# Performance work log

Measured on AMD Instinct MI355X. Metric: run time of the kernel, lower is better.

The kernel has to match this reference:

```python
import jax, jax.numpy as jnp
import numpy as np

D = 512  # input_size
H = 512  # hidden_size

def _linear_init(key, out_f, in_f):
    k1, k2 = jax.random.split(key)
    bound = 1.0 / np.sqrt(in_f)
    W = jax.random.uniform(k1, (out_f, in_f), minval=-bound, maxval=bound, dtype=jnp.float32)
    b = jax.random.uniform(k2, (out_f,), minval=-bound, maxval=bound, dtype=jnp.float32)
    return W, b

def setup_inputs() -> dict:
    key = jax.random.key(0)
    ks = jax.random.split(key, 7)
    x = jax.random.normal(ks[0], (64, 2048, D), dtype=jnp.float32)
    W_ir, b_ir = _linear_init(ks[1], H, D)
    W_hr, b_hr = _linear_init(ks[2], H, H)
    W_iz, b_iz = _linear_init(ks[3], H, D)
    W_hz, b_hz = _linear_init(ks[4], H, H)
    W_in, b_in = _linear_init(ks[5], H, D)
    W_hn, b_hn = _linear_init(ks[6], H, H)
    return {"x": x,
            "W_ir": W_ir, "b_ir": b_ir, "W_hr": W_hr, "b_hr": b_hr,
            "W_iz": W_iz, "b_iz": b_iz, "W_hz": W_hz, "b_hz": b_hz,
            "W_in": W_in, "b_in": b_in, "W_hn": W_hn, "b_hn": b_hn}

def reference(x, W_ir, b_ir, W_hr, b_hr, W_iz, b_iz, W_hz, b_hz, W_in, b_in, W_hn, b_hn):
    B = x.shape[0]
    # Batch all input-side projections across timesteps as big GEMMs: [S,B,H]
    xr = jnp.einsum('bsd,hd->sbh', x, W_ir) + b_ir
    xz = jnp.einsum('bsd,hd->sbh', x, W_iz) + b_iz
    xn = jnp.einsum('bsd,hd->sbh', x, W_in) + b_in

    h0 = jnp.zeros((B, H), dtype=x.dtype)  # torch uses [1,H] zeros; broadcast-equivalent

    def step(h, xs):
        xr_t, xz_t, xn_t = xs
        r = jax.nn.sigmoid(xr_t + h @ W_hr.T + b_hr)
        z = jax.nn.sigmoid(xz_t + h @ W_hz.T + b_hz)
        n = jnp.tanh(xn_t + r * (h @ W_hn.T + b_hn))
        h_new = (1.0 - z) * n + z * h
        return h_new, h_new

    h_last, output = jax.lax.scan(step, h0, (xr, xz, xn))
    return output, h_last  # output: [S,B,H], h_last: [B,H]
```

## Files before the change

### kernel.cpp

```cpp
#include <hip/hip_runtime.h>

#define S_ 2048
#define B_ 64
#define D_ 512
#define H_ 512
#define BH_ (B_*H_)
#define NMEM 8

typedef __attribute__((ext_vector_type(4))) float fx4;
typedef __attribute__((ext_vector_type(8))) short sx8;
typedef __attribute__((ext_vector_type(4))) unsigned int ux4;
typedef __attribute__((ext_vector_type(2))) unsigned int ux2;

__device__ __forceinline__ unsigned short f2bf(float f) {
    union { float f; unsigned int u; } v; v.f = f;
    return (unsigned short)((v.u + 0x7fffu + ((v.u >> 16) & 1u)) >> 16);
}
__device__ __forceinline__ float bf2f(unsigned short b) {
    union { float f; unsigned int u; } v; v.u = ((unsigned int)b) << 16;
    return v.f;
}
__device__ __forceinline__ unsigned int cvtpk(float a, float b) {
    unsigned int r;
    asm("v_cvt_pk_bf16_f32 %0, %1, %2" : "=v"(r) : "v"(a), "v"(b));
    return r;
}

#define BAR() asm volatile("s_waitcnt lgkmcnt(0)\n\ts_barrier" ::: "memory")

__global__ __launch_bounds__(256) void proj_k(
    const float* __restrict__ x,
    const float* __restrict__ Wir, const float* __restrict__ bir,
    const float* __restrict__ Wiz, const float* __restrict__ biz,
    const float* __restrict__ Win, const float* __restrict__ bin_,
    unsigned short* __restrict__ outp_u16,
    unsigned short* __restrict__ xn)
{
    const int nt   = blockIdx.x;
    const int gate = nt >> 2;
    const float* W  = (gate == 0) ? Wir : ((gate == 1) ? Wiz : Win);
    const float* bi = (gate == 0) ? bir : ((gate == 1) ? biz : bin_);
    const int jbase = (nt & 3) * 128;
    const int m0 = blockIdx.y * 128;
    const int t0 = blockIdx.y * 2;

    __shared__ __align__(16) unsigned short As[128][88];
    __shared__ __align__(16) unsigned short Bs[128][88];

    const int tid  = threadIdx.x;
    const int lane = tid & 63;
    const int wv   = tid >> 6;
    const int wm   = wv >> 1, wn = wv & 1;

    fx4 z4 = {0.f, 0.f, 0.f, 0.f};
    fx4 acc[4][4];
#pragma unroll
    for (int i = 0; i < 4; ++i)
#pragma unroll
        for (int j = 0; j < 4; ++j) acc[i][j] = z4;

    const int rr = tid >> 4;
    const int c4 = (tid & 15) * 4;

    for (int kb = 0; kb < 8; ++kb) {
        const int k0 = kb * 64;
#pragma unroll
        for (int pass = 0; pass < 8; ++pass) {
            const int r = pass * 16 + rr;
            const int bb = r & 63, tt = t0 + (r >> 6);
            const float* srcA = x + ((size_t)bb * S_ + tt) * D_ + k0 + c4;
            fx4 va = *(const fx4*)srcA;
            ux2 pa; pa.x = cvtpk(va.x, va.y); pa.y = cvtpk(va.z, va.w);
            *(ux2*)&As[r][c4] = pa;
            const float* srcB = W + (size_t)(jbase + r) * D_ + k0 + c4;
            fx4 vb = *(const fx4*)srcB;
            ux2 pb; pb.x = cvtpk(vb.x, vb.y); pb.y = cvtpk(vb.z, vb.w);
            *(ux2*)&Bs[r][c4] = pb;
        }
        __syncthreads();
#pragma unroll
        for (int kk = 0; kk < 64; kk += 32) {
            const int kloc = kk + (lane >> 4) * 8;
            sx8 af[4], bfv[4];
#pragma unroll
            for (int i = 0; i < 4; ++i)
                af[i] = *(const sx8*)&As[wm * 64 + i * 16 + (lane & 15)][kloc];
#pragma unroll
            for (int i = 0; i < 4; ++i)
                bfv[i] = *(const sx8*)&Bs[wn * 64 + i * 16 + (lane & 15)][kloc];
#pragma unroll
            for (int mi = 0; mi < 4; ++mi)
#pragma unroll
                for (int ni = 0; ni < 4; ++ni)
                    acc[mi][ni] = __builtin_amdgcn_mfma_f32_16x16x32_bf16(
                        af[mi], bfv[ni], acc[mi][ni], 0, 0, 0);
        }
        __syncthreads();
    }

    const int cold = lane & 15;
    const int rowq = (lane >> 4) * 4;
#pragma unroll
    for (int ni = 0; ni < 4; ++ni) {
        const int J = jbase + wn * 64 + ni * 16 + cold;
        const float bb = bi[J];
#pragma unroll
        for (int mi = 0; mi < 4; ++mi) {
#pragma unroll
            for (int reg = 0; reg < 4; ++reg) {
                const int R = m0 + wm * 64 + mi * 16 + rowq + reg;
                const int t = R >> 6, b = R & 63;
                const float val = acc[mi][ni][reg] + bb;
                const size_t e = (size_t)t * BH_ + (size_t)b * H_ + J;
                if (gate < 2) outp_u16[e * 2 + gate] = f2bf(val);
                else          xn[e] = f2bf(val);
            }
        }
    }
}

__global__ __launch_bounds__(256, 1) void gru_k(
    float* out,
    const unsigned short* __restrict__ xn,
    unsigned int* pkt,
    const float* __restrict__ Whr, const float* __restrict__ bhr,
    const float* __restrict__ Whz, const float* __restrict__ bhz,
    const float* __restrict__ Whn, const float* __restrict__ bhn)
{
    const int tid = threadIdx.x, lane = tid & 63, wv = tid >> 6;
    const int bid = blockIdx.x;
    const int g = bid & 15, m = bid >> 4;
    const int c0 = m * 64;
    const int r = lane >> 4;
    const int jcol = c0 + wv * 16 + (lane & 15);
    const int mp = lane >> 3, s7 = lane & 7;

    __shared__ __align__(16) unsigned short hst[2][2048];
    for (int i = tid; i < 4096; i += 256) (&hst[0][0])[i] = 0;

    const int kbase = (lane >> 4) * 8;
    sx8 wfr[16], wfz[16], wfn[16];
#pragma unroll
    for (int kc = 0; kc < 16; ++kc) {
        const int k0 = kc * 32 + kbase;
        const float* pr = Whr + (size_t)jcol * H_ + k0;
        const float* pz = Whz + (size_t)jcol * H_ + k0;
        const float* pn = Whn + (size_t)jcol * H_ + k0;
        sx8 fr, fz, fn;
#pragma unroll
        for (int q = 0; q < 8; ++q) {
            fr[q] = (short)f2bf(pr[q]);
            fz[q] = (short)f2bf(pz[q]);
            fn[q] = (short)f2bf(pn[q]);
        }
        wfr[kc] = fr; wfz[kc] = fz; wfn[kc] = fn;
    }
    const float bhr_v = bhr[jcol], bhz_v = bhz[jcol], bhn_v = bhn[jcol];

    const size_t xoff = (size_t)(4 * g + r) * H_ + jcol;
    unsigned int   xz_c  = __float_as_uint(out[xoff]);
    unsigned short xnn_c = xn[xoff];
    float hprev = 0.f;
    __syncthreads();

    for (int t = 0; t < S_; ++t) {
        const int p1 = (t - 1) & 1, p0 = t & 1;

        if (t > 0 && mp != m) {
            const unsigned int ex = (unsigned int)(t - 1);
            const char* pb = (const char*)pkt +
                ((((size_t)(p1 * 64 + 4 * g + wv)) * NMEM + mp) * 256
                 + (size_t)s7 * 32);
            ux4 q0, q1;
            for (;;) {
                asm volatile(
                    "global_load_dwordx4 %0, %2, off sc0 sc1\n\t"
                    "global_load_dwordx4 %1, %2, off offset:16 sc0 sc1\n\t"
                    "s_waitcnt vmcnt(0)"
                    : "=&v"(q0), "=&v"(q1) : "v"(pb) : "memory");
                if ((((q0.x ^ ex) | (q0.w ^ ex)) |
                     ((q1.x ^ ex) | (q1.w ^ ex))) == 0u) break;
            }
            const int unit = (mp * 2 + (s7 >> 2)) * 16 + wv * 4 + (s7 & 3);
            ux4 w; w.x = q0.y; w.y = q0.z; w.z = q1.y; w.w = q1.z;
            *(ux4*)&hst[p1][unit * 8] = w;
        }

        unsigned int xz_n = xz_c; unsigned short xnn_n = xnn_c;
        if (t + 1 < S_) {
            xz_n  = __float_as_uint(out[(size_t)(t + 1) * BH_ + xoff]);
            xnn_n = xn[(size_t)(t + 1) * BH_ + xoff];
        }
        BAR();

        fx4 ar = {0.f,0.f,0.f,0.f}, az = {0.f,0.f,0.f,0.f}, an = {0.f,0.f,0.f,0.f};
#pragma unroll
        for (int kc = 0; kc < 16; ++kc) {
            sx8 a = *(const sx8*)&hst[p1][(kc * 16 + (lane & 3) * 4 + (lane >> 4)) * 8];
            ar = __builtin_amdgcn_mfma_f32_16x16x32_bf16(a, wfr[kc], ar, 0, 0, 0);
            az = __builtin_amdgcn_mfma_f32_16x16x32_bf16(a, wfz[kc], az, 0, 0, 0);
            an = __builtin_amdgcn_mfma_f32_16x16x32_bf16(a, wfn[kc], an, 0, 0, 0);
        }
        const float sr = (r == 0) ? ar[0] : (r == 1) ? ar[1] : (r == 2) ? ar[2] : ar[3];
        const float sz = (r == 0) ? az[0] : (r == 1) ? az[1] : (r == 2) ? az[2] : az[3];
        const float sn = (r == 0) ? an[0] : (r == 1) ? an[1] : (r == 2) ? an[2] : an[3];
        const float arx = sr + bf2f((unsigned short)(xz_c & 0xffffu)) + bhr_v;
        const float azx = sz + bf2f((unsigned short)(xz_c >> 16)) + bhz_v;
        const float rg = 1.f / (1.f + __expf(-arx));
        const float zg = 1.f / (1.f + __expf(-azx));
        const float nn = tanhf(bf2f(xnn_c) + rg * (sn + bhn_v));
        const float hv = (1.f - zg) * nn + zg * hprev;
        hprev = hv;

        {
            const unsigned int hu1 = (unsigned int)__builtin_amdgcn_mov_dpp(
                (int)__float_as_uint(hv), 0xB1, 0xF, 0xF, true);
            const unsigned int pk01 = cvtpk(hv, __uint_as_float(hu1));
            const unsigned int pk23 = (unsigned int)__builtin_amdgcn_mov_dpp(
                (int)pk01, 0x4E, 0xF, 0xF, true);
            if ((lane & 3) == 0) {
                const int qg = wv * 4 + ((lane & 15) >> 2);
                const unsigned int tag = (unsigned int)t;
                ux4 pk4; pk4.x = tag; pk4.y = pk01; pk4.z = pk23; pk4.w = tag;
                char* addr = (char*)pkt +
                    ((((size_t)(p0 * 64 + 4 * g + r)) * NMEM + m) * 256
                     + (size_t)qg * 16);
                asm volatile("global_store_dwordx4 %0, %1, off sc0 sc1"
                             :: "v"(addr), "v"(pk4) : "memory");
            }
        }
        {
            const int unit = ((jcol >> 5) << 4) + r * 4 + ((jcol >> 3) & 3);
            hst[p0][unit * 8 + (jcol & 7)] = f2bf(hv);
        }
        out[(size_t)t * BH_ + xoff] = hv;
        if (t == S_ - 1) out[(size_t)S_ * BH_ + xoff] = hv;
        xz_c = xz_n; xnn_c = xnn_n;
    }
}

extern "C" void kernel_launch(void* const* d_in, const int* in_sizes, int n_in,
                              void* d_out, int out_size, void* d_ws, size_t ws_size,
                              hipStream_t stream) {
    (void)in_sizes; (void)n_in; (void)out_size; (void)ws_size;
    const float* x    = (const float*)d_in[0];
    const float* Wir  = (const float*)d_in[1];
    const float* bir  = (const float*)d_in[2];
    const float* Whr  = (const float*)d_in[3];
    const float* bhr  = (const float*)d_in[4];
    const float* Wiz  = (const float*)d_in[5];
    const float* biz  = (const float*)d_in[6];
    const float* Whz  = (const float*)d_in[7];
    const float* bhz  = (const float*)d_in[8];
    const float* Win  = (const float*)d_in[9];
    const float* bin_ = (const float*)d_in[10];
    const float* Whn  = (const float*)d_in[11];
    const float* bhn  = (const float*)d_in[12];

    unsigned short* xn = (unsigned short*)d_ws;
    unsigned int* pkt = (unsigned int*)((char*)d_ws + (size_t)S_ * BH_ * 2);

    proj_k<<<dim3(12, 1024, 1), 256, 0, stream>>>(
        x, Wir, bir, Wiz, biz, Win, bin_, (unsigned short*)d_out, xn);
    gru_k<<<dim3(128, 1, 1), 256, 0, stream>>>(
        (float*)d_out, xn, pkt, Whr, bhr, Whz, bhz, Whn, bhn);
}
```

Measured before the change: 3.972 ms.

## Fuse input projection and GRU recurrence into one kernel with per-tile ready flags

Merges the projection GEMM and the persistent GRU recurrence into one launch. The first 128 blocks run the recurrence and the remaining blocks compute projection tiles, each publishing a magic-value flag when its tile is written. Recurrence blocks poll these flags, prefetching the next timestep's flags, so they can start while later projection tiles are still being computed. This overlaps the projection with the serial scan, at the cost of flag polling and a memset, and it depends on the 128 recurrence blocks being co-resident and scheduled first.

```diff
diff --git a/kernel.cpp b/kernel.cpp
--- a/kernel.cpp
+++ b/kernel.cpp
@@ -6,6 +6,8 @@
 #define H_ 512
 #define BH_ (B_*H_)
 #define NMEM 8
+#define NGRU 128
+#define MGK 0xC0DE600Du
 
 typedef __attribute__((ext_vector_type(4))) float fx4;
 typedef __attribute__((ext_vector_type(8))) short sx8;
@@ -28,114 +30,125 @@
 
 #define BAR() asm volatile("s_waitcnt lgkmcnt(0)\n\ts_barrier" ::: "memory")
 
-__global__ __launch_bounds__(256) void proj_k(
+#define ALL12(a,b,c) ((((a.x^MGK)|(a.y^MGK)|(a.z^MGK)|(a.w^MGK)) | \
+                       ((b.x^MGK)|(b.y^MGK)|(b.z^MGK)|(b.w^MGK)) | \
+                       ((c.x^MGK)|(c.y^MGK)|(c.z^MGK)|(c.w^MGK))) == 0u)
+
+__global__ __launch_bounds__(256, 1) void fused_k(
     const float* __restrict__ x,
     const float* __restrict__ Wir, const float* __restrict__ bir,
     const float* __restrict__ Wiz, const float* __restrict__ biz,
     const float* __restrict__ Win, const float* __restrict__ bin_,
-    unsigned short* __restrict__ outp_u16,
-    unsigned short* __restrict__ xn)
+    const float* __restrict__ Whr, const float* __restrict__ bhr,
+    const float* __restrict__ Whz, const float* __restrict__ bhz,
+    const float* __restrict__ Whn, const float* __restrict__ bhn,
+    float* out, unsigned short* xn, unsigned int* pkt, unsigned int* xflag)
 {
-    const int nt   = blockIdx.x;
-    const int gate = nt >> 2;
-    const float* W  = (gate == 0) ? Wir : ((gate == 1) ? Wiz : Win);
-    const float* bi = (gate == 0) ? bir : ((gate == 1) ? biz : bin_);
-    const int jbase = (nt & 3) * 128;
-    const int m0 = blockIdx.y * 128;
-    const int t0 = blockIdx.y * 2;
-
     __shared__ __align__(16) unsigned short As[128][88];
     __shared__ __align__(16) unsigned short Bs[128][88];
+    __shared__ __align__(16) unsigned short hst[2][2048];
 
     const int tid  = threadIdx.x;
+    const int bid  = blockIdx.x;
     const int lane = tid & 63;
     const int wv   = tid >> 6;
-    const int wm   = wv >> 1, wn = wv & 1;
-
-    fx4 z4 = {0.f, 0.f, 0.f, 0.f};
-    fx4 acc[4][4];
-#pragma unroll
-    for (int i = 0; i < 4; ++i)
-#pragma unroll
-        for (int j = 0; j < 4; ++j) acc[i][j] = z4;
-
-    const int rr = tid >> 4;
-    const int c4 = (tid & 15) * 4;
-
-    for (int kb = 0; kb < 8; ++kb) {
-        const int k0 = kb * 64;
-#pragma unroll
-        for (int pass = 0; pass < 8; ++pass) {
-            const int r = pass * 16 + rr;
-            const int bb = r & 63, tt = t0 + (r >> 6);
-            const float* srcA = x + ((size_t)bb * S_ + tt) * D_ + k0 + c4;
-            fx4 va = *(const fx4*)srcA;
-            ux2 pa; pa.x = cvtpk(va.x, va.y); pa.y = cvtpk(va.z, va.w);
-            *(ux2*)&As[r][c4] = pa;
-            const float* srcB = W + (size_t)(jbase + r) * D_ + k0 + c4;
-            fx4 vb = *(const fx4*)srcB;
-            ux2 pb; pb.x = cvtpk(vb.x, vb.y); pb.y = cvtpk(vb.z, vb.w);
-            *(ux2*)&Bs[r][c4] = pb;
+
+    if (bid >= NGRU) {
+        const int pb   = bid - NGRU;
+        const int nt   = pb % 12;
+        const int Y    = pb / 12;
+        const int gate = nt >> 2;
+        const float* W  = (gate == 0) ? Wir : ((gate == 1) ? Wiz : Win);
+        const float* bi = (gate == 0) ? bir : ((gate == 1) ? biz : bin_);
+        const int jbase = (nt & 3) * 128;
+        const int m0 = Y * 128;
+        const int t0 = Y * 2;
+
+        const int wm = wv >> 1, wn = wv & 1;
+
+        fx4 z4 = {0.f, 0.f, 0.f, 0.f};
+        fx4 acc[4][4];
+#pragma unroll
+        for (int i = 0; i < 4; ++i)
+#pragma unroll
+            for (int j = 0; j < 4; ++j) acc[i][j] = z4;
+
+        const int rr = tid >> 4;
+        const int c4 = (tid & 15) * 4;
+
+        for (int kb = 0; kb < 8; ++kb) {
+            const int k0 = kb * 64;
+#pragma unroll
+            for (int pass = 0; pass < 8; ++pass) {
+                const int r = pass * 16 + rr;
+                const int bb = r & 63, tt = t0 + (r >> 6);
+                const float* srcA = x + ((size_t)bb * S_ + tt) * D_ + k0 + c4;
+                fx4 va = *(const fx4*)srcA;
+                ux2 pa; pa.x = cvtpk(va.x, va.y); pa.y = cvtpk(va.z, va.w);
+                *(ux2*)&As[r][c4] = pa;
+                const float* srcB = W + (size_t)(jbase + r) * D_ + k0 + c4;
+                fx4 vb = *(const fx4*)srcB;
+                ux2 pb2; pb2.x = cvtpk(vb.x, vb.y); pb2.y = cvtpk(vb.z, vb.w);
+                *(ux2*)&Bs[r][c4] = pb2;
+            }
+            __syncthreads();
+#pragma unroll
+            for (int kk = 0; kk < 64; kk += 32) {
+                const int kloc = kk + (lane >> 4) * 8;
+                sx8 af[4], bfv[4];
+#pragma unroll
+                for (int i = 0; i < 4; ++i)
+                    af[i] = *(const sx8*)&As[wm * 64 + i * 16 + (lane & 15)][kloc];
+#pragma unroll
+                for (int i = 0; i < 4; ++i)
+                    bfv[i] = *(const sx8*)&Bs[wn * 64 + i * 16 + (lane & 15)][kloc];
+#pragma unroll
+                for (int mi = 0; mi < 4; ++mi)
+#pragma unroll
+                    for (int ni = 0; ni < 4; ++ni)
+                        acc[mi][ni] = __builtin_amdgcn_mfma_f32_16x16x32_bf16(
+                            af[mi], bfv[ni], acc[mi][ni], 0, 0, 0);
+            }
+            __syncthreads();
+        }
+
+        unsigned short* outp_u16 = (unsigned short*)out;
+        const int cold = lane & 15;
+        const int rowq = (lane >> 4) * 4;
+#pragma unroll
+        for (int ni = 0; ni < 4; ++ni) {
+            const int J = jbase + wn * 64 + ni * 16 + cold;
+            const float bb = bi[J];
+#pragma unroll
+            for (int mi = 0; mi < 4; ++mi) {
+#pragma unroll
+                for (int reg = 0; reg < 4; ++reg) {
+                    const int R = m0 + wm * 64 + mi * 16 + rowq + reg;
+                    const int t = R >> 6, b = R & 63;
+                    const float val = acc[mi][ni][reg] + bb;
+                    const size_t e = (size_t)t * BH_ + (size_t)b * H_ + J;
+                    if (gate < 2) outp_u16[e * 2 + gate] = f2bf(val);
+                    else          xn[e] = f2bf(val);
+                }
+            }
         }
         __syncthreads();
-#pragma unroll
-        for (int kk = 0; kk < 64; kk += 32) {
-            const int kloc = kk + (lane >> 4) * 8;
-            sx8 af[4], bfv[4];
-#pragma unroll
-            for (int i = 0; i < 4; ++i)
-                af[i] = *(const sx8*)&As[wm * 64 + i * 16 + (lane & 15)][kloc];
-#pragma unroll
-            for (int i = 0; i < 4; ++i)
-                bfv[i] = *(const sx8*)&Bs[wn * 64 + i * 16 + (lane & 15)][kloc];
-#pragma unroll
-            for (int mi = 0; mi < 4; ++mi)
-#pragma unroll
-                for (int ni = 0; ni < 4; ++ni)
-                    acc[mi][ni] = __builtin_amdgcn_mfma_f32_16x16x32_bf16(
-                        af[mi], bfv[ni], acc[mi][ni], 0, 0, 0);
-        }
-        __syncthreads();
+        if (tid == 0) {
+            __threadfence();
+            unsigned int mg = MGK;
+            unsigned int* fa = xflag + (size_t)Y * 12 + nt;
+            asm volatile("global_store_dword %0, %1, off sc0 sc1"
+                         :: "v"(fa), "v"(mg) : "memory");
+        }
+        return;
     }
 
-    const int cold = lane & 15;
-    const int rowq = (lane >> 4) * 4;
-#pragma unroll
-    for (int ni = 0; ni < 4; ++ni) {
-        const int J = jbase + wn * 64 + ni * 16 + cold;
-        const float bb = bi[J];
-#pragma unroll
-        for (int mi = 0; mi < 4; ++mi) {
-#pragma unroll
-            for (int reg = 0; reg < 4; ++reg) {
-                const int R = m0 + wm * 64 + mi * 16 + rowq + reg;
-                const int t = R >> 6, b = R & 63;
-                const float val = acc[mi][ni][reg] + bb;
-                const size_t e = (size_t)t * BH_ + (size_t)b * H_ + J;
-                if (gate < 2) outp_u16[e * 2 + gate] = f2bf(val);
-                else          xn[e] = f2bf(val);
-            }
-        }
-    }
-}
-
-__global__ __launch_bounds__(256, 1) void gru_k(
-    float* out,
-    const unsigned short* __restrict__ xn,
-    unsigned int* pkt,
-    const float* __restrict__ Whr, const float* __restrict__ bhr,
-    const float* __restrict__ Whz, const float* __restrict__ bhz,
-    const float* __restrict__ Whn, const float* __restrict__ bhn)
-{
-    const int tid = threadIdx.x, lane = tid & 63, wv = tid >> 6;
-    const int bid = blockIdx.x;
     const int g = bid & 15, m = bid >> 4;
     const int c0 = m * 64;
     const int r = lane >> 4;
     const int jcol = c0 + wv * 16 + (lane & 15);
     const int mp = lane >> 3, s7 = lane & 7;
 
-    __shared__ __align__(16) unsigned short hst[2][2048];
     for (int i = tid; i < 4096; i += 256) (&hst[0][0])[i] = 0;
 
     const int kbase = (lane >> 4) * 8;
@@ -156,6 +169,23 @@
         wfr[kc] = fr; wfz[kc] = fz; wfn[kc] = fn;
     }
     const float bhr_v = bhr[jcol], bhz_v = bhz[jcol], bhn_v = bhn[jcol];
+
+    ux4 fr0 = {0,0,0,0}, fr1 = {0,0,0,0}, fr2 = {0,0,0,0};
+    int Ymax = 0;
+
+    {
+        const unsigned int* f0 = xflag;
+        for (;;) {
+            asm volatile(
+                "global_load_dwordx4 %0, %3, off sc0 sc1\n\t"
+                "global_load_dwordx4 %1, %3, off offset:16 sc0 sc1\n\t"
+                "global_load_dwordx4 %2, %3, off offset:32 sc0 sc1\n\t"
+                "s_waitcnt vmcnt(0)"
+                : "=&v"(fr0), "=&v"(fr1), "=&v"(fr2) : "v"(f0) : "memory");
+            if (ALL12(fr0, fr1, fr2)) break;
+            __builtin_amdgcn_s_sleep(8);
+        }
+    }
 
     const size_t xoff = (size_t)(4 * g + r) * H_ + jcol;
     unsigned int   xz_c  = __float_as_uint(out[xoff]);
@@ -185,11 +215,38 @@
             ux4 w; w.x = q0.y; w.y = q0.z; w.z = q1.y; w.w = q1.z;
             *(ux4*)&hst[p1][unit * 8] = w;
         }
+        asm volatile("s_waitcnt vmcnt(0)"
+                     : "+v"(fr0), "+v"(fr1), "+v"(fr2) :: "memory");
 
         unsigned int xz_n = xz_c; unsigned short xnn_n = xnn_c;
         if (t + 1 < S_) {
+            const int Y1 = (t + 1) >> 1;
+            if (Y1 > Ymax) {
+                if (!ALL12(fr0, fr1, fr2)) {
+                    const unsigned int* fp1 = xflag + (size_t)Y1 * 12;
+                    for (;;) {
+                        asm volatile(
+                            "global_load_dwordx4 %0, %3, off sc0 sc1\n\t"
+                            "global_load_dwordx4 %1, %3, off offset:16 sc0 sc1\n\t"
+                            "global_load_dwordx4 %2, %3, off offset:32 sc0 sc1\n\t"
+                            "s_waitcnt vmcnt(0)"
+                            : "=&v"(fr0), "=&v"(fr1), "=&v"(fr2)
+                            : "v"(fp1) : "memory");
+                        if (ALL12(fr0, fr1, fr2)) break;
+                        __builtin_amdgcn_s_sleep(2);
+                    }
+                }
+                Ymax = Y1;
+            }
             xz_n  = __float_as_uint(out[(size_t)(t + 1) * BH_ + xoff]);
             xnn_n = xn[(size_t)(t + 1) * BH_ + xoff];
+            const int Yf = (Y1 + 1 < 1024) ? Y1 + 1 : 1023;
+            const unsigned int* fpn = xflag + (size_t)Yf * 12;
+            asm volatile(
+                "global_load_dwordx4 %0, %3, off sc0 sc1\n\t"
+                "global_load_dwordx4 %1, %3, off offset:16 sc0 sc1\n\t"
+                "global_load_dwordx4 %2, %3, off offset:32 sc0 sc1"
+                : "=&v"(fr0), "=&v"(fr1), "=&v"(fr2) : "v"(fpn) : "memory");
         }
         BAR();
 
@@ -258,10 +315,14 @@
     const float* bhn  = (const float*)d_in[12];
 
     unsigned short* xn = (unsigned short*)d_ws;
-    unsigned int* pkt = (unsigned int*)((char*)d_ws + (size_t)S_ * BH_ * 2);
-
-    proj_k<<<dim3(12, 1024, 1), 256, 0, stream>>>(
-        x, Wir, bir, Wiz, biz, Win, bin_, (unsigned short*)d_out, xn);
-    gru_k<<<dim3(128, 1, 1), 256, 0, stream>>>(
-        (float*)d_out, xn, pkt, Whr, bhr, Whz, bhz, Whn, bhn);
-}
+    char* base = (char*)d_ws + (size_t)S_ * BH_ * 2;
+    unsigned int* pkt   = (unsigned int*)base;
+    unsigned int* xflag = (unsigned int*)(base + 256 * 1024);
+
+    hipMemsetAsync(xflag, 0, 12 * 1024 * sizeof(unsigned int), stream);
+
+    fused_k<<<dim3(NGRU + 12 * 1024, 1, 1), 256, 0, stream>>>(
+        x, Wir, bir, Wiz, biz, Win, bin_,
+        Whr, bhr, Whz, bhz, Whn, bhn,
+        (float*)d_out, xn, pkt, xflag);
+}
```

Measured after the change: 3.856 ms. 2.9% less time.
